# Kernel tuning notes

Hardware: AMD Instinct MI355X
Metric: run time of the kernel (lower is better)

## Reference

```python
import jax, jax.numpy as jnp
import numpy as np

B, T, C = 2, 2048, 2048
N_HEADS, N_KV_HEADS = 16, 4
HEAD_DIM = C // N_HEADS  # 128
NUM_GROUPS = N_HEADS // N_KV_HEADS  # 4


def setup_inputs() -> dict:
    key = jax.random.key(0)
    ks = jax.random.split(key, 5)
    s = 1.0 / np.sqrt(C)
    return {
        "x": jax.random.normal(ks[0], (B, T, C), dtype=jnp.float32),
        "Wq": jax.random.normal(ks[1], (C, N_HEADS * HEAD_DIM), dtype=jnp.float32) * s,
        "Wk": jax.random.normal(ks[2], (C, N_KV_HEADS * HEAD_DIM), dtype=jnp.float32) * s,
        "Wv": jax.random.normal(ks[3], (C, N_KV_HEADS * HEAD_DIM), dtype=jnp.float32) * s,
        "Wo": jax.random.normal(ks[4], (C, C), dtype=jnp.float32) * s,
    }


def _rope_tables(seq_len, head_dim, dtype):
    theta = 1.0 / (10000.0 ** (jnp.arange(0, head_dim, 2, dtype=jnp.float32) / head_dim))
    freqs = jnp.arange(seq_len, dtype=jnp.float32)[:, None] * theta[None, :]  # [T, hd/2]
    cos = jnp.concatenate([jnp.cos(freqs), jnp.cos(freqs)], axis=-1)  # [T, hd]
    sin = jnp.concatenate([jnp.sin(freqs), jnp.sin(freqs)], axis=-1)
    return cos.astype(dtype), sin.astype(dtype)


def _rotate_half(x):
    x1, x2 = jnp.split(x, 2, axis=-1)
    return jnp.concatenate([-x2, x1], axis=-1)


def reference(x, Wq, Wk, Wv, Wo):
    b, t, c = x.shape
    q = (x @ Wq).reshape(b, t, N_HEADS, HEAD_DIM).transpose(0, 2, 1, 3)      # [B,H,T,hd]
    k = (x @ Wk).reshape(b, t, N_KV_HEADS, HEAD_DIM).transpose(0, 2, 1, 3)   # [B,Hkv,T,hd]
    v = (x @ Wv).reshape(b, t, N_KV_HEADS, HEAD_DIM).transpose(0, 2, 1, 3)

    cos, sin = _rope_tables(t, HEAD_DIM, x.dtype)  # [T,hd]
    cos = cos[None, None]  # [1,1,T,hd]
    sin = sin[None, None]
    q = q * cos + _rotate_half(q) * sin
    k = k * cos + _rotate_half(k) * sin

    # GQA: expand kv heads (repeat_interleave along head dim)
    k = jnp.repeat(k, NUM_GROUPS, axis=1)  # [B,H,T,hd]
    v = jnp.repeat(v, NUM_GROUPS, axis=1)

    scale = 1.0 / jnp.sqrt(jnp.asarray(HEAD_DIM, dtype=x.dtype))
    scores = jnp.einsum("bhqd,bhkd->bhqk", q, k) * scale  # [B,H,T,T]
    causal = jnp.tril(jnp.ones((t, t), dtype=bool))
    scores = jnp.where(causal[None, None], scores, jnp.asarray(-jnp.inf, dtype=scores.dtype))
    attn = jax.nn.softmax(scores, axis=-1)
    out = jnp.einsum("bhqk,bhkd->bhqd", attn, v)  # [B,H,T,hd]
    out = out.transpose(0, 2, 1, 3).reshape(b, t, c)
    return out @ Wo
```

## Files before the change

### kernel.cpp

```cpp
#include <hip/hip_runtime.h>
#include <hip/hip_bf16.h>
#include <math.h>

typedef __hip_bfloat16 bf16;
typedef __attribute__((ext_vector_type(8))) short bf16x8;
typedef __attribute__((ext_vector_type(4))) float floatx4;

__device__ __forceinline__ void async_copy16(const bf16* g, bf16* l) {
    __builtin_amdgcn_global_load_lds(
        (__attribute__((address_space(1))) void*)(void*)g,
        (__attribute__((address_space(3))) void*)(void*)l,
        16, 0, 0);
}

template <int N>
__device__ __forceinline__ void wait_vm_bar() {
    if constexpr (N == 0) asm volatile("s_waitcnt vmcnt(0)\n\ts_barrier" ::: "memory");
    else if constexpr (N == 1) asm volatile("s_waitcnt vmcnt(1)\n\ts_barrier" ::: "memory");
    else if constexpr (N == 2) asm volatile("s_waitcnt vmcnt(2)\n\ts_barrier" ::: "memory");
    else if constexpr (N == 3) asm volatile("s_waitcnt vmcnt(3)\n\ts_barrier" ::: "memory");
    else if constexpr (N == 4) asm volatile("s_waitcnt vmcnt(4)\n\ts_barrier" ::: "memory");
    else if constexpr (N == 5) asm volatile("s_waitcnt vmcnt(5)\n\ts_barrier" ::: "memory");
    else if constexpr (N == 6) asm volatile("s_waitcnt vmcnt(6)\n\ts_barrier" ::: "memory");
    else if constexpr (N == 7) asm volatile("s_waitcnt vmcnt(7)\n\ts_barrier" ::: "memory");
    else if constexpr (N == 8) asm volatile("s_waitcnt vmcnt(8)\n\ts_barrier" ::: "memory");
}

__global__ __launch_bounds__(256) void prep_kernel(const float* __restrict__ x,
                                                   bf16* __restrict__ xb,
                                                   const float* __restrict__ Wq,
                                                   const float* __restrict__ Wk,
                                                   const float* __restrict__ Wv,
                                                   const float* __restrict__ Wo,
                                                   bf16* __restrict__ Wt,
                                                   bf16* __restrict__ Wot) {
    const int tid = threadIdx.x;
    int bid = blockIdx.x;
    if (bid < 8192) {
        int i = bid * 256 + tid;
        float4 v = ((const float4*)x)[i];
        union { ushort4 u; bf16 b[4]; } o;
        o.b[0] = __float2bfloat16(v.x);
        o.b[1] = __float2bfloat16(v.y);
        o.b[2] = __float2bfloat16(v.z);
        o.b[3] = __float2bfloat16(v.w);
        ((ushort4*)xb)[i] = o.u;
        return;
    }
    bid -= 8192;
    __shared__ float tile[32][33];
    const float* in;
    bf16* out;
    int N, bx, by;
    if (bid < 4096)      { in = Wq; out = Wt;               N = 2048; bx = bid & 63; by = bid >> 6; }
    else if (bid < 5120) { int b2 = bid - 4096; in = Wk; out = Wt + 2048 * 2048; N = 512; bx = b2 & 15; by = b2 >> 4; }
    else if (bid < 6144) { int b2 = bid - 5120; in = Wv; out = Wt + 2560 * 2048; N = 512; bx = b2 & 15; by = b2 >> 4; }
    else                 { int b2 = bid - 6144; in = Wo; out = Wot;              N = 2048; bx = b2 & 63; by = b2 >> 6; }
    const int K = 2048;
    const int nb = bx * 32, kb = by * 32;
    const int tx = tid & 31, ty = tid >> 5;
    for (int j = ty; j < 32; j += 8)
        tile[j][tx] = in[(size_t)(kb + j) * N + nb + tx];
    __syncthreads();
    for (int j = ty; j < 32; j += 8)
        out[(size_t)(nb + j) * K + kb + tx] = __float2bfloat16(tile[tx][j]);
}

__global__ __launch_bounds__(512) void gemm256(const bf16* __restrict__ A,
                                               const bf16* __restrict__ Bt,
                                               bf16* __restrict__ C,
                                               int M, int N, int K) {
    __shared__ bf16 As[4][256 * 32];
    __shared__ bf16 Bs[4][256 * 32];
    const int tid = threadIdx.x;
    const int wave = tid >> 6, lane = tid & 63;
    const int c = lane & 15, quad = lane >> 4;
    const int wm = wave >> 2, wn = wave & 3;
    const int mBase = blockIdx.y * 256, nBase = blockIdx.x * 256;
    const int rdOff = (quad ^ ((c >> 1) & 3)) << 3;

    const bf16* gAs[2];
    const bf16* gBs[2];
#pragma unroll
    for (int i = 0; i < 2; i++) {
        int ci = i * 512 + tid;
        int r = ci >> 2;
        int sc = (ci & 3) ^ ((r >> 1) & 3);
        gAs[i] = A + (size_t)(mBase + r) * K + sc * 8;
        gBs[i] = Bt + (size_t)(nBase + r) * K + sc * 8;
    }
    const int ldsW = wave * 512;

    floatx4 acc[8][4];
#pragma unroll
    for (int mt = 0; mt < 8; mt++)
#pragma unroll
        for (int nt = 0; nt < 4; nt++) acc[mt][nt] = (floatx4){0.f, 0.f, 0.f, 0.f};

    auto stage_half = [&](int t, int i) {
        const int bb = t & 3;
        const int lo = i * 4096 + ldsW;
        async_copy16(gAs[i] + (size_t)t * 32, &As[bb][0] + lo);
        async_copy16(gBs[i] + (size_t)t * 32, &Bs[bb][0] + lo);
    };

    auto tile_body = [&](int t, bool doStage) {
        const int bb = t & 3;
        const bf16* as = &As[bb][0];
        const bf16* bs = &Bs[bb][0];
        bf16x8 bfr[4], af[4];
#pragma unroll
        for (int nt = 0; nt < 4; nt++)
            bfr[nt] = *(const bf16x8*)(bs + (wn * 64 + nt * 16 + c) * 32 + rdOff);
#pragma unroll
        for (int mt = 0; mt < 4; mt++)
            af[mt] = *(const bf16x8*)(as + (wm * 128 + mt * 16 + c) * 32 + rdOff);
        if (doStage) stage_half(t + 3, 0);
        __builtin_amdgcn_s_setprio(1);
#pragma unroll
        for (int mt = 0; mt < 4; mt++)
#pragma unroll
            for (int nt = 0; nt < 4; nt++)
                acc[mt][nt] = __builtin_amdgcn_mfma_f32_16x16x32_bf16(af[mt], bfr[nt],
                                                                      acc[mt][nt], 0, 0, 0);
        __builtin_amdgcn_s_setprio(0);
#pragma unroll
        for (int mt = 0; mt < 4; mt++)
            af[mt] = *(const bf16x8*)(as + (wm * 128 + 64 + mt * 16 + c) * 32 + rdOff);
        if (doStage) stage_half(t + 3, 1);
        __builtin_amdgcn_s_setprio(1);
#pragma unroll
        for (int mt = 0; mt < 4; mt++)
#pragma unroll
            for (int nt = 0; nt < 4; nt++)
                acc[4 + mt][nt] = __builtin_amdgcn_mfma_f32_16x16x32_bf16(af[mt], bfr[nt],
                                                                          acc[4 + mt][nt], 0, 0, 0);
        __builtin_amdgcn_s_setprio(0);
    };

    const int NT = K >> 5;
    stage_half(0, 0); stage_half(0, 1);
    stage_half(1, 0); stage_half(1, 1);
    stage_half(2, 0); stage_half(2, 1);
    wait_vm_bar<8>();

    for (int t = 0; t < NT - 3; ++t) {
        tile_body(t, true);
        wait_vm_bar<8>();
    }
    tile_body(NT - 3, false);
    wait_vm_bar<4>();
    tile_body(NT - 2, false);
    wait_vm_bar<0>();
    tile_body(NT - 1, false);

#pragma unroll
    for (int mt = 0; mt < 8; mt++)
#pragma unroll
        for (int nt = 0; nt < 4; nt++)
#pragma unroll
            for (int r = 0; r < 4; r++) {
                int row = mBase + wm * 128 + mt * 16 + quad * 4 + r;
                int col = nBase + wn * 64 + nt * 16 + c;
                C[(size_t)row * N + col] = __float2bfloat16(acc[mt][nt][r]);
            }
}

template <int BM, int BN, bool OUTF32>
__global__ __launch_bounds__(512) void gemm256g(const bf16* __restrict__ A,
                                                const bf16* __restrict__ Bt,
                                                void* __restrict__ Cout,
                                                int M, int N, int K) {
    constexpr int CA = BM * 4;
    constexpr int CB = BN * 4;
    constexpr int A_LPT = CA / 512;
    constexpr int EXTRA = CB - 512;
    constexpr int WM = BM / 2, WN = BN / 4;
    constexpr int MT = WM / 16, NT = WN / 16;
    __shared__ bf16 As[4][BM * 32];
    __shared__ bf16 Bs[4][BN * 32];
    const int tid = threadIdx.x;
    const int wave = tid >> 6, lane = tid & 63;
    const int c = lane & 15, quad = lane >> 4;
    const int wm = wave >> 2, wn = wave & 3;

    const int GX = gridDim.x;
    const int GB = GX * gridDim.y;
    int bid = blockIdx.y * GX + blockIdx.x;
    bid = (bid & 7) * (GB >> 3) + (bid >> 3);
    const int mBase = (bid / GX) * BM, nBase = (bid % GX) * BN;

    const int rdOff = (quad ^ ((c >> 1) & 3)) << 3;
    const bool heavy = (EXTRA == 512) ? true : (tid < EXTRA);

    const bf16* gA[A_LPT];
#pragma unroll
    for (int s = 0; s < A_LPT; s++) {
        int ci = s * 512 + tid;
        int r = ci >> 2;
        int sc = (ci & 3) ^ ((r >> 1) & 3);
        gA[s] = A + (size_t)(mBase + r) * K + sc * 8;
    }
    const bf16* gB0;
    {
        int r = tid >> 2;
        int sc = (tid & 3) ^ ((r >> 1) & 3);
        gB0 = Bt + (size_t)(nBase + r) * K + sc * 8;
    }
    const bf16* gB1 = nullptr;
    if (heavy) {
        int ci = 512 + tid;
        int r = ci >> 2;
        int sc = (ci & 3) ^ ((r >> 1) & 3);
        gB1 = Bt + (size_t)(nBase + r) * K + sc * 8;
    }

    floatx4 acc[MT][NT];
#pragma unroll
    for (int mt = 0; mt < MT; mt++)
#pragma unroll
        for (int nt = 0; nt < NT; nt++) acc[mt][nt] = (floatx4){0.f, 0.f, 0.f, 0.f};

    auto stage_a = [&](int t) {
        const int bb = t & 3;
#pragma unroll
        for (int s = 0; s < A_LPT; s++)
            async_copy16(gA[s] + (size_t)t * 32, &As[bb][(s * 512 + tid) * 8]);
    };
    auto stage_b = [&](int t) {
        const int bb = t & 3;
        async_copy16(gB0 + (size_t)t * 32, &Bs[bb][tid * 8]);
        if (heavy) async_copy16(gB1 + (size_t)t * 32, &Bs[bb][(512 + tid) * 8]);
    };
    auto boundary = [&]() {
        if (heavy) wait_vm_bar<A_LPT + 2>();
        else       wait_vm_bar<A_LPT + 1>();
    };

    auto tile_body = [&](int t, bool doStage) {
        const int bb = t & 3;
        const bf16* as = &As[bb][0];
        const bf16* bs = &Bs[bb][0];
        bf16x8 bfr[NT], af[MT / 2];
#pragma unroll
        for (int nt = 0; nt < NT; nt++)
            bfr[nt] = *(const bf16x8*)(bs + (wn * WN + nt * 16 + c) * 32 + rdOff);
#pragma unroll
        for (int mt = 0; mt < MT / 2; mt++)
            af[mt] = *(const bf16x8*)(as + (wm * WM + mt * 16 + c) * 32 + rdOff);
        if (doStage) stage_a(t + 2);
        __builtin_amdgcn_s_setprio(1);
#pragma unroll
        for (int mt = 0; mt < MT / 2; mt++)
#pragma unroll
            for (int nt = 0; nt < NT; nt++)
                acc[mt][nt] = __builtin_amdgcn_mfma_f32_16x16x32_bf16(af[mt], bfr[nt],
                                                                      acc[mt][nt], 0, 0, 0);
        __builtin_amdgcn_s_setprio(0);
#pragma unroll
        for (int mt = 0; mt < MT / 2; mt++)
            af[mt] = *(const bf16x8*)(as + (wm * WM + (MT / 2 + mt) * 16 + c) * 32 + rdOff);
        if (doStage) stage_b(t + 2);
        __builtin_amdgcn_s_setprio(1);
#pragma unroll
        for (int mt = 0; mt < MT / 2; mt++)
#pragma unroll
            for (int nt = 0; nt < NT; nt++)
                acc[MT / 2 + mt][nt] = __builtin_amdgcn_mfma_f32_16x16x32_bf16(
                    af[mt], bfr[nt], acc[MT / 2 + mt][nt], 0, 0, 0);
        __builtin_amdgcn_s_setprio(0);
    };

    const int NTK = K >> 5;
    stage_a(0); stage_b(0);
    stage_a(1); stage_b(1);
    boundary();

    for (int t = 0; t < NTK - 2; ++t) {
        tile_body(t, true);
        boundary();
    }
    tile_body(NTK - 2, false);
    wait_vm_bar<0>();
    tile_body(NTK - 1, false);

#pragma unroll
    for (int mt = 0; mt < MT; mt++)
#pragma unroll
        for (int nt = 0; nt < NT; nt++)
#pragma unroll
            for (int r = 0; r < 4; r++) {
                int row = mBase + wm * WM + mt * 16 + quad * 4 + r;
                int col = nBase + wn * WN + nt * 16 + c;
                if (OUTF32)
                    ((float*)Cout)[(size_t)row * N + col] = acc[mt][nt][r];
                else
                    ((bf16*)Cout)[(size_t)row * N + col] = __float2bfloat16(acc[mt][nt][r]);
            }
}

__global__ __launch_bounds__(256) void rope_vtrans(bf16* __restrict__ QKV,
                                                   bf16* __restrict__ Vtg) {
    const int tid = threadIdx.x;
    int bid = blockIdx.x;
    if (bid < 4096) {
        int idx = bid * 256 + tid;
        int d = idx & 63;
        int h = (idx >> 6) & 3;
        int row = idx >> 8;
        int t = row & 2047;
        float theta = exp2f(-(float)d * 0.20762050593045827f);
        float ang = (float)t * theta;
        float sv, cv;
        __sincosf(ang, &sv, &cv);
        bf16* p = QKV + 2048 + (size_t)row * 3072 + h * 128 + d;
        float x1 = __bfloat162float(p[0]);
        float x2 = __bfloat162float(p[64]);
        p[0]  = __float2bfloat16(x1 * cv - x2 * sv);
        p[64] = __float2bfloat16(x2 * cv + x1 * sv);
        return;
    }
    bid -= 4096;
    __shared__ bf16 tile[32][34];
    const int bx = bid & 63, by = (bid >> 6) & 3, bh = bid >> 8;
    const int b = bh >> 2, kvh = bh & 3;
    const int t0 = bx * 32, d0 = by * 32;
    const bf16* src = QKV + (size_t)b * 2048 * 3072 + 2560 + kvh * 128;
    const int tx = tid & 31, ty = tid >> 5;
    for (int j = ty; j < 32; j += 8)
        tile[j][tx] = src[(size_t)(t0 + j) * 3072 + d0 + tx];
    __syncthreads();
    bf16* dst = Vtg + (size_t)bh * 128 * 2048;
    const int g = tx >> 2;
    const int txp = (((g & 3) << 1) | (g >> 2)) * 4 + (tx & 3);
    for (int j = ty; j < 32; j += 8)
        dst[(size_t)(d0 + j) * 2048 + t0 + txp] = tile[tx][j];
}

__global__ __launch_bounds__(256, 4) void flash_attn5(const bf16* __restrict__ QKV,
                                                      const bf16* __restrict__ Vtg,
                                                      bf16* __restrict__ Slot0,
                                                      bf16* __restrict__ Slot1,
                                                      float* __restrict__ Ls) {
    const int T = 2048, STR = 3072;
    __shared__ bf16 Ks[4 * 64 * 32];
    __shared__ bf16 Vs[2 * 128 * 32];
    const int b = blockIdx.z, h = blockIdx.y;
    const int pj = blockIdx.x >> 1, s = blockIdx.x & 1;
    const int kvh = h >> 2;
    const int tid = threadIdx.x, wave = tid >> 6, lane = tid & 63;
    const int c = lane & 15, quad = lane >> 4;
    const float C2 = 0.12751541717525597f;

    const bf16* Kg = QKV + (size_t)b * T * STR + 2048 + kvh * 128;
    const bf16* Vg = Vtg + (size_t)(b * 4 + kvh) * 128 * 2048;
    const int srow = tid >> 2;
    const int xcol = ((tid & 3) ^ ((tid >> 3) & 3)) << 3;
    const int koff = (quad ^ ((c >> 1) & 3)) << 3;
    const int qa = 31 - pj;

    auto run_part = [&](int qtile, int ktlo, int kthi, bf16* slot, int lsSlot) {
        const int q0 = qtile * 64;
        bf16x8 qf[4];
        {
            const bf16* qp = QKV + ((size_t)b * T + q0 + wave * 16 + c) * STR + h * 128 + quad * 8;
#pragma unroll
            for (int ks = 0; ks < 4; ks++) qf[ks] = *(const bf16x8*)(qp + ks * 32);
            const float t = (float)(q0 + wave * 16 + c);
#pragma unroll
            for (int ks = 0; ks < 2; ks++)
#pragma unroll
                for (int j = 0; j < 8; j++) {
                    int d = ks * 32 + quad * 8 + j;
                    float theta = exp2f((float)d * -0.20762050593045827f);
                    float sv, cv;
                    __sincosf(t * theta, &sv, &cv);
                    float lo = __bfloat162float(((const bf16*)&qf[ks])[j]);
                    float hi = __bfloat162float(((const bf16*)&qf[ks + 2])[j]);
                    ((bf16*)&qf[ks])[j]     = __float2bfloat16((lo * cv - hi * sv) * C2);
                    ((bf16*)&qf[ks + 2])[j] = __float2bfloat16((hi * cv + lo * sv) * C2);
                }
        }
        floatx4 accO[8];
#pragma unroll
        for (int nt = 0; nt < 8; nt++) accO[nt] = (floatx4){0.f, 0.f, 0.f, 0.f};
        float lsum = 0.f;

        for (int kt = ktlo; kt < kthi; kt++) {
            const int kt0 = kt * 64;
#pragma unroll
            for (int it = 0; it < 4; it++) {
                async_copy16(Kg + (size_t)(kt0 + srow) * STR + it * 32 + xcol,
                             Ks + it * 2048 + wave * 512);
                async_copy16(Vg + (size_t)((it & 1) * 64 + srow) * 2048 + kt0 + (it >> 1) * 32 + xcol,
                             Vs + it * 2048 + wave * 512);
            }
            __syncthreads();
            floatx4 sf[4];
#pragma unroll
            for (int nt = 0; nt < 4; nt++) sf[nt] = (floatx4){0.f, 0.f, 0.f, 0.f};
#pragma unroll
            for (int ks = 0; ks < 4; ks++)
#pragma unroll
                for (int nt = 0; nt < 4; nt++) {
                    bf16x8 kf = *(const bf16x8*)(Ks + ks * 2048 + (nt * 16 + c) * 32 + koff);
                    sf[nt] = __builtin_amdgcn_mfma_f32_16x16x32_bf16(kf, qf[ks], sf[nt], 0, 0, 0);
                }
            if (kt == qtile) {
                const int qrel = wave * 16 + c;
#pragma unroll
                for (int nt = 0; nt < 4; nt++)
#pragma unroll
                    for (int r = 0; r < 4; r++) {
                        float p = exp2f(sf[nt][r]);
                        if (nt * 16 + quad * 4 + r > qrel) p = 0.f;
                        lsum += p;
                        sf[nt][r] = p;
                    }
            } else {
#pragma unroll
                for (int nt = 0; nt < 4; nt++)
#pragma unroll
                    for (int r = 0; r < 4; r++) {
                        float p = exp2f(sf[nt][r]);
                        lsum += p;
                        sf[nt][r] = p;
                    }
            }
#pragma unroll
            for (int kc = 0; kc < 2; kc++) {
                bf16x8 pf;
#pragma unroll
                for (int j = 0; j < 4; j++) {
                    ((bf16*)&pf)[j]     = __float2bfloat16(sf[2 * kc][j]);
                    ((bf16*)&pf)[4 + j] = __float2bfloat16(sf[2 * kc + 1][j]);
                }
#pragma unroll
                for (int nt = 0; nt < 8; nt++) {
                    bf16x8 vf = *(const bf16x8*)(Vs + kc * 4096 + (nt * 16 + c) * 32 + koff);
                    accO[nt] = __builtin_amdgcn_mfma_f32_16x16x32_bf16(pf, vf, accO[nt], 0, 0, 0);
                }
            }
            __syncthreads();
        }
        {
            float v = lsum;
            v += __shfl_xor(v, 16);
            v += __shfl_xor(v, 32);
            if (quad == 0)
                Ls[(size_t)lsSlot * 65536 + ((size_t)(b * 16 + h) * 32 + qtile) * 64
                   + wave * 16 + c] = v;
        }
        const size_t orow = (size_t)b * T + q0 + wave * 16 + quad * 4;
#pragma unroll
        for (int nt = 0; nt < 8; nt++)
#pragma unroll
            for (int r = 0; r < 4; r++)
                slot[(orow + r) * 2048 + h * 128 + nt * 16 + c] =
                    __float2bfloat16(accO[nt][r]);
    };

    if (s == 0) {
        run_part(qa, 0, 17, Slot0, 0);
    } else {
        run_part(qa, 17, 32 - pj, Slot1, 1);
        run_part(pj, 0, pj + 1, Slot0, 0);
    }
}

__global__ __launch_bounds__(256) void attn_merge(bf16* __restrict__ AO,
                                                  const bf16* __restrict__ P1,
                                                  const float* __restrict__ Ls) {
    int i = blockIdx.x * 256 + threadIdx.x;
    int row = i >> 8;
    int cg = (i & 255) << 3;
    int b = row >> 11, t = row & 2047;
    int qtile = t >> 6;
    int h = cg >> 7;
    size_t off = (size_t)row * 2048 + cg;
    size_t li = ((size_t)(b * 16 + h) * 32 + qtile) * 64 + (t & 63);
    bf16x8 a0 = *(const bf16x8*)(AO + off);
    float l = Ls[li];
    float acc[8];
#pragma unroll
    for (int j = 0; j < 8; j++) acc[j] = __bfloat162float(((const bf16*)&a0)[j]);
    if (qtile >= 16) {
        bf16x8 a1 = *(const bf16x8*)(P1 + off);
        l += Ls[65536 + li];
#pragma unroll
        for (int j = 0; j < 8; j++) acc[j] += __bfloat162float(((const bf16*)&a1)[j]);
    }
    float inv = 1.0f / l;
    bf16x8 o;
#pragma unroll
    for (int j = 0; j < 8; j++) ((bf16*)&o)[j] = __float2bfloat16(acc[j] * inv);
    *(bf16x8*)(AO + off) = o;
}

extern "C" void kernel_launch(void* const* d_in, const int* in_sizes, int n_in,
                              void* d_out, int out_size, void* d_ws, size_t ws_size,
                              hipStream_t stream) {
    const float* x  = (const float*)d_in[0];
    const float* Wq = (const float*)d_in[1];
    const float* Wk = (const float*)d_in[2];
    const float* Wv = (const float*)d_in[3];
    const float* Wo = (const float*)d_in[4];

    char* ws = (char*)d_ws;
    bf16* xb   = (bf16*)(ws);
    bf16* Vtg  = (bf16*)(ws);
    bf16* Slt1 = (bf16*)(ws + 4194304);
    float* Ls  = (float*)(ws + 20971520);
    bf16* Wt   = (bf16*)(ws + 16777216);
    bf16* Wot  = (bf16*)(ws + 29360128);
    bf16* QKV  = (bf16*)(ws + 37748736);
    bf16* AO   = (bf16*)(ws + 62914560);

    prep_kernel<<<18432, 256, 0, stream>>>(x, xb, Wq, Wk, Wv, Wo, Wt, Wot);

    gemm256<<<dim3(12, 16), 512, 0, stream>>>(xb, Wt, QKV, 4096, 3072, 2048);

    rope_vtrans<<<6144, 256, 0, stream>>>(QKV, Vtg);

    flash_attn5<<<dim3(32, 16, 2), 256, 0, stream>>>(QKV, Vtg, AO, Slt1, Ls);

    attn_merge<<<4096, 256, 0, stream>>>(AO, Slt1, Ls);

    gemm256g<128, 256, true><<<dim3(8, 32), 512, 0, stream>>>(AO, Wot, d_out, 4096, 2048, 2048);
}
```

Measured before the change: 298.2 us.

## Restructure QKV GEMM into 8-phase pipeline with 64-wide K steps

Replaces the 4-buffer, 32-wide K pipeline of the QKV projection GEMM with a double-buffered scheme. Each stage covers a 64-wide K step split into two 32-wide halves, with separate A/B staging interleaved across four MFMA phases. Each phase is separated by barriers and lgkmcnt waits, with scheduling barriers to control ordering. The aim is to spread global-to-LDS loads more evenly across the compute phases and hide latency better. The cost is many more barriers per K step, which could stall the waves.

```diff
diff --git a/kernel.cpp b/kernel.cpp
--- a/kernel.cpp
+++ b/kernel.cpp
@@ -20,9 +20,6 @@
     else if constexpr (N == 2) asm volatile("s_waitcnt vmcnt(2)\n\ts_barrier" ::: "memory");
     else if constexpr (N == 3) asm volatile("s_waitcnt vmcnt(3)\n\ts_barrier" ::: "memory");
     else if constexpr (N == 4) asm volatile("s_waitcnt vmcnt(4)\n\ts_barrier" ::: "memory");
-    else if constexpr (N == 5) asm volatile("s_waitcnt vmcnt(5)\n\ts_barrier" ::: "memory");
-    else if constexpr (N == 6) asm volatile("s_waitcnt vmcnt(6)\n\ts_barrier" ::: "memory");
-    else if constexpr (N == 7) asm volatile("s_waitcnt vmcnt(7)\n\ts_barrier" ::: "memory");
     else if constexpr (N == 8) asm volatile("s_waitcnt vmcnt(8)\n\ts_barrier" ::: "memory");
 }
 
@@ -66,12 +63,12 @@
         out[(size_t)(nb + j) * K + kb + tx] = __float2bfloat16(tile[tx][j]);
 }
 
-__global__ __launch_bounds__(512) void gemm256(const bf16* __restrict__ A,
-                                               const bf16* __restrict__ Bt,
-                                               bf16* __restrict__ C,
-                                               int M, int N, int K) {
-    __shared__ bf16 As[4][256 * 32];
-    __shared__ bf16 Bs[4][256 * 32];
+__global__ __launch_bounds__(512) void gemm8p(const bf16* __restrict__ A,
+                                              const bf16* __restrict__ Bt,
+                                              bf16* __restrict__ C,
+                                              int M, int N, int K) {
+    __shared__ bf16 As[2][2][256 * 32];
+    __shared__ bf16 Bs[2][2][256 * 32];
     const int tid = threadIdx.x;
     const int wave = tid >> 6, lane = tid & 63;
     const int c = lane & 15, quad = lane >> 4;
@@ -79,17 +76,16 @@
     const int mBase = blockIdx.y * 256, nBase = blockIdx.x * 256;
     const int rdOff = (quad ^ ((c >> 1) & 3)) << 3;
 
-    const bf16* gAs[2];
-    const bf16* gBs[2];
-#pragma unroll
-    for (int i = 0; i < 2; i++) {
-        int ci = i * 512 + tid;
+    const bf16* gA[2];
+    const bf16* gB[2];
+#pragma unroll
+    for (int l = 0; l < 2; l++) {
+        int ci = l * 512 + tid;
         int r = ci >> 2;
         int sc = (ci & 3) ^ ((r >> 1) & 3);
-        gAs[i] = A + (size_t)(mBase + r) * K + sc * 8;
-        gBs[i] = Bt + (size_t)(nBase + r) * K + sc * 8;
-    }
-    const int ldsW = wave * 512;
+        gA[l] = A + (size_t)(mBase + r) * K + sc * 8;
+        gB[l] = Bt + (size_t)(nBase + r) * K + sc * 8;
+    }
 
     floatx4 acc[8][4];
 #pragma unroll
@@ -97,25 +93,38 @@
 #pragma unroll
         for (int nt = 0; nt < 4; nt++) acc[mt][nt] = (floatx4){0.f, 0.f, 0.f, 0.f};
 
-    auto stage_half = [&](int t, int i) {
-        const int bb = t & 3;
-        const int lo = i * 4096 + ldsW;
-        async_copy16(gAs[i] + (size_t)t * 32, &As[bb][0] + lo);
-        async_copy16(gBs[i] + (size_t)t * 32, &Bs[bb][0] + lo);
-    };
-
-    auto tile_body = [&](int t, bool doStage) {
-        const int bb = t & 3;
-        const bf16* as = &As[bb][0];
-        const bf16* bs = &Bs[bb][0];
-        bf16x8 bfr[4], af[4];
+    auto stageA = [&](int t, int ks) {
+        bf16* dst = &As[t & 1][ks][0];
+#pragma unroll
+        for (int l = 0; l < 2; l++)
+            async_copy16(gA[l] + (size_t)t * 64 + ks * 32, dst + (l * 512 + tid) * 8);
+    };
+    auto stageB = [&](int t, int ks) {
+        bf16* dst = &Bs[t & 1][ks][0];
+#pragma unroll
+        for (int l = 0; l < 2; l++)
+            async_copy16(gB[l] + (size_t)t * 64 + ks * 32, dst + (l * 512 + tid) * 8);
+    };
+
+    bf16x8 bfr[4], af[4];
+    auto readB = [&](int s, int ks) {
+        const bf16* bs = &Bs[s & 1][ks][0];
 #pragma unroll
         for (int nt = 0; nt < 4; nt++)
             bfr[nt] = *(const bf16x8*)(bs + (wn * 64 + nt * 16 + c) * 32 + rdOff);
+    };
+    auto readA = [&](int s, int ks, int half) {
+        const bf16* as = &As[s & 1][ks][0];
 #pragma unroll
         for (int mt = 0; mt < 4; mt++)
-            af[mt] = *(const bf16x8*)(as + (wm * 128 + mt * 16 + c) * 32 + rdOff);
-        if (doStage) stage_half(t + 3, 0);
+            af[mt] = *(const bf16x8*)(as + (wm * 128 + half * 64 + mt * 16 + c) * 32 + rdOff);
+    };
+    auto mid_sync = [&]() {
+        __builtin_amdgcn_s_barrier();
+        asm volatile("s_waitcnt lgkmcnt(0)" ::: "memory");
+        __builtin_amdgcn_sched_barrier(0);
+    };
+    auto mfma_lo = [&]() {
         __builtin_amdgcn_s_setprio(1);
 #pragma unroll
         for (int mt = 0; mt < 4; mt++)
@@ -124,10 +133,8 @@
                 acc[mt][nt] = __builtin_amdgcn_mfma_f32_16x16x32_bf16(af[mt], bfr[nt],
                                                                       acc[mt][nt], 0, 0, 0);
         __builtin_amdgcn_s_setprio(0);
-#pragma unroll
-        for (int mt = 0; mt < 4; mt++)
-            af[mt] = *(const bf16x8*)(as + (wm * 128 + 64 + mt * 16 + c) * 32 + rdOff);
-        if (doStage) stage_half(t + 3, 1);
+    };
+    auto mfma_hi = [&]() {
         __builtin_amdgcn_s_setprio(1);
 #pragma unroll
         for (int mt = 0; mt < 4; mt++)
@@ -138,21 +145,33 @@
         __builtin_amdgcn_s_setprio(0);
     };
 
-    const int NT = K >> 5;
-    stage_half(0, 0); stage_half(0, 1);
-    stage_half(1, 0); stage_half(1, 1);
-    stage_half(2, 0); stage_half(2, 1);
+    const int NT = K >> 6;
+    stageA(0, 0); stageB(0, 0); stageA(0, 1); stageB(0, 1);
+    stageA(1, 0); stageB(1, 0);
     wait_vm_bar<8>();
 
-    for (int t = 0; t < NT - 3; ++t) {
-        tile_body(t, true);
-        wait_vm_bar<8>();
-    }
-    tile_body(NT - 3, false);
-    wait_vm_bar<4>();
-    tile_body(NT - 2, false);
-    wait_vm_bar<0>();
-    tile_body(NT - 1, false);
+    for (int s = 0; s < NT; ++s) {
+        const bool st1 = (s + 1 < NT), st2 = (s + 2 < NT);
+        readB(s, 0); readA(s, 0, 0);
+        if (st1) stageA(s + 1, 1);
+        mid_sync(); mfma_lo();
+        __builtin_amdgcn_s_barrier();
+        readA(s, 0, 1);
+        if (st1) stageB(s + 1, 1);
+        mid_sync(); mfma_hi();
+        if (st1) wait_vm_bar<8>();
+        else     wait_vm_bar<0>();
+        readB(s, 1); readA(s, 1, 0);
+        if (st2) stageA(s + 2, 0);
+        mid_sync(); mfma_lo();
+        __builtin_amdgcn_s_barrier();
+        readA(s, 1, 1);
+        if (st2) stageB(s + 2, 0);
+        mid_sync(); mfma_hi();
+        if (st2)      wait_vm_bar<8>();
+        else if (st1) wait_vm_bar<4>();
+        else          __builtin_amdgcn_s_barrier();
+    }
 
 #pragma unroll
     for (int mt = 0; mt < 8; mt++)
@@ -518,7 +537,7 @@
 
     prep_kernel<<<18432, 256, 0, stream>>>(x, xb, Wq, Wk, Wv, Wo, Wt, Wot);
 
-    gemm256<<<dim3(12, 16), 512, 0, stream>>>(xb, Wt, QKV, 4096, 3072, 2048);
+    gemm8p<<<dim3(12, 16), 512, 0, stream>>>(xb, Wt, QKV, 4096, 3072, 2048);
 
     rope_vtrans<<<6144, 256, 0, stream>>>(QKV, Vtg);
 
```

Measured after the change: 303.7 us. No clear change (+1.9%).
